# Performance work log

Hardware: AMD Instinct MI355X
Metric: run time of the kernel (lower is better)

## Reference

```python
import jax, jax.numpy as jnp
import numpy as np

B, N, DIM = 16, 1024, 768
H, HD = 12, 64  # num_heads, head_dim


def rotate_half(x):
    x1, x2 = jnp.split(x, 2, axis=-1)
    return jnp.concatenate((-x2, x1), axis=-1)


def setup_inputs() -> dict:
    key = jax.random.key(0)
    k1, k2, k3, k4, k5 = jax.random.split(key, 5)
    x = jax.random.normal(k1, (B, N, DIM), dtype=jnp.float32)
    # precomputed 2D-RoPE angles for the 32x32 patch grid: (N, head_dim)
    sin = jax.random.uniform(k2, (N, HD), dtype=jnp.float32, minval=-1.0, maxval=1.0)
    cos = jax.random.uniform(k3, (N, HD), dtype=jnp.float32, minval=-1.0, maxval=1.0)
    # params: qkv (no bias), proj (with bias)
    W_qkv = jax.random.normal(k4, (DIM, 3 * H * HD), dtype=jnp.float32) / np.sqrt(DIM)
    W_proj = jax.random.normal(k5, (H * HD, DIM), dtype=jnp.float32) / np.sqrt(H * HD)
    b_proj = jnp.zeros((DIM,), dtype=jnp.float32)
    return {"x": x, "sin": sin, "cos": cos, "W_qkv": W_qkv, "W_proj": W_proj, "b_proj": b_proj}


def reference(x, sin, cos, W_qkv, W_proj, b_proj):
    b, n, _ = x.shape
    qkv = (x @ W_qkv).reshape(b, n, 3, H, HD)
    q, k, v = jnp.moveaxis(qkv, 2, 0)          # each (b, n, H, HD)
    q = jnp.swapaxes(q, 1, 2)                  # (b, H, n, HD)
    k = jnp.swapaxes(k, 1, 2)
    v = jnp.swapaxes(v, 1, 2)
    # RoPE (prefix_tokens=0: apply to all tokens); sin/cos broadcast (n,HD)->(1,1,n,HD)
    s = sin[None, None]
    c = cos[None, None]
    q = q * c + rotate_half(q) * s
    k = k * c + rotate_half(k) * s
    # scaled dot-product attention (non-causal, no mask, no dropout)
    scale = 1.0 / jnp.sqrt(jnp.asarray(HD, dtype=q.dtype))
    scores = jnp.einsum('bhqd,bhkd->bhqk', q, k) * scale
    attn = jax.nn.softmax(scores, axis=-1)
    out = jnp.einsum('bhqk,bhkd->bhqd', attn, v)
    out = jnp.swapaxes(out, 1, 2).reshape(b, n, H * HD)
    return out @ W_proj + b_proj
```

## Files before the change

### kernel.cpp

```cpp
#include <hip/hip_runtime.h>


typedef __attribute__((ext_vector_type(8))) _Float16 fp16x8;
typedef __attribute__((ext_vector_type(4))) _Float16 h4;
typedef __attribute__((ext_vector_type(4))) float f32x4;

#define MFMA16(a, b, c) __builtin_amdgcn_mfma_f32_16x16x32_f16(a, b, c, 0, 0, 0)

__device__ __forceinline__ float fexp2(float x) {
    float r;
    asm volatile("v_exp_f32 %0, %1\n\ts_nop 0" : "=v"(r) : "v"(x));
    return r;
}

__device__ __forceinline__ void gload16(const _Float16* g, _Float16* s) {
    __builtin_amdgcn_global_load_lds(
        (const __attribute__((address_space(1))) unsigned int*)g,
        (__attribute__((address_space(3))) unsigned int*)s, 16, 0, 0);
}

__global__ __launch_bounds__(256) void tofp16_kernel(const float* __restrict__ in,
                                                     _Float16* __restrict__ outp, int n4) {
    int i = blockIdx.x * 256 + threadIdx.x;
    if (i >= n4) return;
    float4 v = ((const float4*)in)[i];
    h4 o;
    o[0] = (_Float16)v.x;
    o[1] = (_Float16)v.y;
    o[2] = (_Float16)v.z;
    o[3] = (_Float16)v.w;
    *(h4*)(outp + (size_t)i * 4) = o;
}

__global__ __launch_bounds__(256) void ttrans_kernel(const float* __restrict__ W,
                                                     _Float16* __restrict__ outp,
                                                     int rows, int cols) {
    __shared__ float tile[32][33];
    const int c0 = blockIdx.x * 32, r0 = blockIdx.y * 32;
    const int t = threadIdx.x;
#pragma unroll
    for (int i = 0; i < 4; ++i) {
        int idx = t + i * 256;
        int r = idx >> 5, c = idx & 31;
        tile[r][c] = W[(size_t)(r0 + r) * cols + c0 + c];
    }
    __syncthreads();
#pragma unroll
    for (int i = 0; i < 4; ++i) {
        int idx = t + i * 256;
        int rp = idx >> 5, cp = idx & 31;
        outp[(size_t)(c0 + rp) * rows + r0 + cp] = (_Float16)tile[cp][rp];
    }
}

__global__ __launch_bounds__(256) void ropetab_kernel(const float* __restrict__ sinp,
                                                      const float* __restrict__ cosp,
                                                      float4* __restrict__ tab) {
    int idx = blockIdx.x * 256 + threadIdx.x;
    int n = idx >> 5, d = idx & 31;
    float4 v;
    v.x = cosp[n * 64 + d];
    v.y = sinp[n * 64 + d];
    v.z = cosp[n * 64 + d + 32];
    v.w = sinp[n * 64 + d + 32];
    tab[idx] = v;
}

template <bool SWAP>
__device__ __forceinline__ void gemm_core8(
    const _Float16* __restrict__ Ag, const _Float16* __restrict__ Bg,
    _Float16* lds, int m0, int n0, f32x4 (&acc)[4][4]) {
    constexpr int BUF = 12288;
    constexpr int OB = 8192;
    const int t = threadIdx.x, l = t & 63, w = t >> 6;
    const int wr = w >> 1, wc = w & 1;
    const int hi = l >> 4, qL = l & 15;

    const int scol = ((t & 3) ^ ((t >> 3) & 3)) << 3;
    const int srow = t >> 2;

    int afo[4], bfo[4];
#pragma unroll
    for (int i = 0; i < 4; ++i) {
        int r = wr * 64 + i * 16 + qL;
        afo[i] = r * 32 + ((hi ^ ((r >> 1) & 3)) << 3);
        int c = wc * 64 + i * 16 + qL;
        bfo[i] = OB + c * 32 + ((hi ^ ((c >> 1) & 3)) << 3);
    }

    auto stageA = [&](int kt, int b) {
        _Float16* base = lds + b * BUF;
        const int k0 = kt * 32;
        gload16(Ag + (size_t)(m0 + srow) * 768 + k0 + scol,
                base + (w * 16) * 32);
        gload16(Ag + (size_t)(m0 + 128 + srow) * 768 + k0 + scol,
                base + (128 + w * 16) * 32);
    };
    auto stageB = [&](int kt, int b) {
        _Float16* base = lds + b * BUF;
        const int k0 = kt * 32;
        gload16(Bg + (size_t)(n0 + srow) * 768 + k0 + scol,
                base + OB + (w * 16) * 32);
    };

    stageA(0, 0);
    stageB(0, 0);
    stageA(1, 1);
    stageB(1, 1);
    asm volatile("s_waitcnt vmcnt(3)" ::: "memory");
    __builtin_amdgcn_s_barrier();

    for (int kt = 0; kt < 24; ++kt) {
        const int bn = (kt + 2) % 3;
        _Float16* bb = lds + (kt % 3) * BUF;

        if (kt < 22) stageA(kt + 2, bn);
        fp16x8 af[4], bf[4];
#pragma unroll
        for (int j = 0; j < 4; ++j) bf[j] = *(const fp16x8*)(bb + bfo[j]);
#pragma unroll
        for (int i = 0; i < 2; ++i) af[i] = *(const fp16x8*)(bb + afo[i]);
        __builtin_amdgcn_s_barrier();
        asm volatile("s_waitcnt lgkmcnt(0)" ::: "memory");
        __builtin_amdgcn_s_setprio(1);
#pragma unroll
        for (int i = 0; i < 2; ++i)
#pragma unroll
            for (int j = 0; j < 4; ++j) {
                if constexpr (SWAP)
                    acc[i][j] = MFMA16(bf[j], af[i], acc[i][j]);
                else
                    acc[i][j] = MFMA16(af[i], bf[j], acc[i][j]);
            }
        __builtin_amdgcn_s_setprio(0);
        __builtin_amdgcn_s_barrier();

        if (kt < 22) stageB(kt + 2, bn);
#pragma unroll
        for (int i = 2; i < 4; ++i) af[i] = *(const fp16x8*)(bb + afo[i]);
        __builtin_amdgcn_s_barrier();
        asm volatile("s_waitcnt lgkmcnt(0)" ::: "memory");
        __builtin_amdgcn_s_setprio(1);
#pragma unroll
        for (int i = 2; i < 4; ++i)
#pragma unroll
            for (int j = 0; j < 4; ++j) {
                if constexpr (SWAP)
                    acc[i][j] = MFMA16(bf[j], af[i], acc[i][j]);
                else
                    acc[i][j] = MFMA16(af[i], bf[j], acc[i][j]);
            }
        __builtin_amdgcn_s_setprio(0);

        if (kt < 22)
            asm volatile("s_waitcnt vmcnt(3)" ::: "memory");
        else
            asm volatile("s_waitcnt vmcnt(0)" ::: "memory");
        __builtin_amdgcn_s_barrier();
    }
}

__global__ __launch_bounds__(512, 4) void qkv_qk_gemm(
    const _Float16* __restrict__ Ag, const _Float16* __restrict__ Bg,
    const float4* __restrict__ tab, _Float16* __restrict__ Qf,
    _Float16* __restrict__ Kf) {
    __shared__ _Float16 lds[3 * 12288];
    const int t = threadIdx.x, l = t & 63, w = t >> 6;
    const int wr = w >> 1, wc = w & 1;
    const int hi = l >> 4, qL = l & 15;

    const int bid = blockIdx.x;
    const int xcd = bid & 7, local = bid >> 3;
    const int m0 = (xcd * 8 + (local & 7)) * 256;
    const int n0 = (local >> 3) * 128;

    f32x4 acc[4][4];
#pragma unroll
    for (int i = 0; i < 4; ++i)
#pragma unroll
        for (int j = 0; j < 4; ++j) acc[i][j] = (f32x4){0.f, 0.f, 0.f, 0.f};

    gemm_core8<true>(Ag, Bg, lds, m0, n0, acc);

    const int colbase = n0 + wc * 64;
    const int sector = colbase / 768;
    const int h = (colbase % 768) >> 6;
    _Float16* dst = (sector == 0) ? Qf : Kf;
    const float SC = (sector == 0) ? 0.18033688011f : 1.0f;

#pragma unroll
    for (int ms = 0; ms < 4; ++ms) {
        int m = m0 + wr * 64 + ms * 16 + qL;
        int b = m >> 10, n = m & 1023;
        size_t base = ((size_t)(b * 12 + h) * 1024 + n) * 64;
#pragma unroll
        for (int ns = 0; ns < 2; ++ns) {
            int d0 = ns * 16 + hi * 4;
            h4 lo4, hi4;
#pragma unroll
            for (int reg = 0; reg < 4; ++reg) {
                int d = d0 + reg;
                float4 cs = tab[n * 32 + d];
                float vlo = acc[ms][ns][reg], vhi = acc[ms][ns + 2][reg];
                lo4[reg] = (_Float16)((vlo * cs.x - vhi * cs.y) * SC);
                hi4[reg] = (_Float16)((vhi * cs.z + vlo * cs.w) * SC);
            }
            *(h4*)(dst + base + d0) = lo4;
            *(h4*)(dst + base + d0 + 32) = hi4;
        }
    }
}

__global__ __launch_bounds__(512, 4) void qkv_v_gemm(
    const _Float16* __restrict__ Ag, const _Float16* __restrict__ Bg,
    _Float16* __restrict__ Vt) {
    __shared__ _Float16 lds[3 * 12288];
    const int t = threadIdx.x, l = t & 63, w = t >> 6;
    const int wr = w >> 1, wc = w & 1;
    const int hi = l >> 4, qL = l & 15;

    const int bid = blockIdx.x;
    const int xcd = bid & 7, local = bid >> 3;
    const int m0 = (xcd * 8 + (local & 7)) * 256;
    const int n0 = (12 + (local >> 3)) * 128;

    f32x4 acc[4][4];
#pragma unroll
    for (int i = 0; i < 4; ++i)
#pragma unroll
        for (int j = 0; j < 4; ++j) acc[i][j] = (f32x4){0.f, 0.f, 0.f, 0.f};

    gemm_core8<false>(Ag, Bg, lds, m0, n0, acc);

    const int h = ((n0 + wc * 64) % 768) >> 6;

#pragma unroll
    for (int ms = 0; ms < 4; ++ms) {
        int mbase = m0 + wr * 64 + ms * 16 + hi * 4;
        int b = mbase >> 10, nb = mbase & 1023;
        int bh = b * 12 + h;
#pragma unroll
        for (int ns = 0; ns < 4; ++ns) {
            int d = ns * 16 + qL;
            h4 pk;
#pragma unroll
            for (int reg = 0; reg < 4; ++reg) pk[reg] = (_Float16)acc[ms][ns][reg];
            *(h4*)(Vt + ((size_t)bh * 64 + d) * 1024 + nb) = pk;
        }
    }
}

__global__ __launch_bounds__(512, 4) void proj_gemm(
    const _Float16* __restrict__ Ag, const _Float16* __restrict__ Bg,
    const float* __restrict__ bias, float* __restrict__ out) {
    __shared__ _Float16 lds[3 * 12288];
    const int t = threadIdx.x, l = t & 63, w = t >> 6;
    const int wr = w >> 1, wc = w & 1;
    const int hi = l >> 4, qL = l & 15;

    const int bid = blockIdx.x;
    const int xcd = bid & 7, local = bid >> 3;
    const int m0 = (xcd * 8 + (local & 7)) * 256;
    const int n0 = (local >> 3) * 128;

    f32x4 acc[4][4];
#pragma unroll
    for (int i = 0; i < 4; ++i)
#pragma unroll
        for (int j = 0; j < 4; ++j) acc[i][j] = (f32x4){0.f, 0.f, 0.f, 0.f};

    gemm_core8<true>(Ag, Bg, lds, m0, n0, acc);

#pragma unroll
    for (int ms = 0; ms < 4; ++ms) {
        int m = m0 + wr * 64 + ms * 16 + qL;
#pragma unroll
        for (int ns = 0; ns < 4; ++ns) {
            int c = n0 + wc * 64 + ns * 16 + hi * 4;
            float4 bv = *(const float4*)(bias + c);
            float4 r;
            r.x = acc[ms][ns][0] + bv.x;
            r.y = acc[ms][ns][1] + bv.y;
            r.z = acc[ms][ns][2] + bv.z;
            r.w = acc[ms][ns][3] + bv.w;
            *(float4*)(out + (size_t)m * 768 + c) = r;
        }
    }
}

__global__ __launch_bounds__(256, 3) void attn_kernel(
    const _Float16* __restrict__ Qf, const _Float16* __restrict__ Kfg,
    const _Float16* __restrict__ Vtg, _Float16* __restrict__ aof) {
    __shared__ _Float16 khs[2][64][64];
    __shared__ _Float16 vts[2][64][64];
    __shared__ _Float16 pbuf[4][32][72];

    const int t = threadIdx.x, l = t & 63, w = t >> 6;
    const int flat = blockIdx.x;
    const int xcd = flat & 7, idx = flat >> 3;
    const int bh = xcd * 24 + (idx >> 3);
    const int n0 = (idx & 7) * 128;
    const int bq = bh / 12, hh = bh % 12;
    const size_t base = (size_t)bh << 16;
    const int hi = l >> 4, qL = l & 15;

    fp16x8 qf[2][2];
#pragma unroll
    for (int q2 = 0; q2 < 2; ++q2)
#pragma unroll
        for (int kk = 0; kk < 2; ++kk) {
            size_t off = base + (size_t)(n0 + w * 32 + q2 * 16 + qL) * 64 +
                         kk * 32 + (hi << 3);
            qf[q2][kk] = *(const fp16x8*)(Qf + off);
        }

    const int r0 = w * 16;
    const int srow = l >> 3;
    const int scol = ((l & 7) ^ srow) << 3;
    const _Float16* kf_src = Kfg + base + (size_t)(r0 + srow) * 64 + scol;
    const _Float16* vt_src = Vtg + base + (size_t)(r0 + srow) * 1024 + scol;

    int kfo[4][2];
#pragma unroll
    for (int c = 0; c < 4; ++c)
#pragma unroll
        for (int kk = 0; kk < 2; ++kk) {
            int row = c * 16 + qL;
            int col16 = (kk << 2) | hi;
            kfo[c][kk] = row * 64 + ((col16 ^ (row & 7)) << 3);
        }

    f32x4 ot[4][2];
    float l_part[2] = {0.f, 0.f};
#pragma unroll
    for (int q2 = 0; q2 < 2; ++q2)
#pragma unroll
        for (int dt = 0; dt < 4; ++dt) ot[dt][q2] = (f32x4){0.f, 0.f, 0.f, 0.f};

    auto stage = [&](int kt, int b) {
        const _Float16* ks = kf_src + (size_t)kt * 4096;
        gload16(ks, &khs[b][r0][0]);
        gload16(ks + 512, &khs[b][r0 + 8][0]);
        const _Float16* vs = vt_src + kt * 64;
        gload16(vs, &vts[b][r0][0]);
        gload16(vs + 8 * 1024, &vts[b][r0 + 8][0]);
    };

    stage(0, 0);
    __syncthreads();

    for (int kt = 0; kt < 16; ++kt) {
        const int cur = kt & 1;
        if (kt < 15) stage(kt + 1, cur ^ 1);

        const _Float16* kb = &khs[cur][0][0];
        const _Float16* vb = &vts[cur][0][0];

        f32x4 s[4][2];
#pragma unroll
        for (int c = 0; c < 4; ++c) {
            fp16x8 kf0 = *(const fp16x8*)(kb + kfo[c][0]);
            fp16x8 kf1 = *(const fp16x8*)(kb + kfo[c][1]);
#pragma unroll
            for (int q2 = 0; q2 < 2; ++q2) {
                f32x4 a = (f32x4){0.f, 0.f, 0.f, 0.f};
                a = MFMA16(kf0, qf[q2][0], a);
                a = MFMA16(kf1, qf[q2][1], a);
                s[c][q2] = a;
            }
        }

#pragma unroll
        for (int q2 = 0; q2 < 2; ++q2) {
            const int prow = q2 * 16 + qL;
            float lsum = 0.f;
#pragma unroll
            for (int c = 0; c < 4; ++c) {
                float p0 = fexp2(s[c][q2][0] - 4.0f);
                float p1 = fexp2(s[c][q2][1] - 4.0f);
                float p2 = fexp2(s[c][q2][2] - 4.0f);
                float p3 = fexp2(s[c][q2][3] - 4.0f);
                lsum += (p0 + p1) + (p2 + p3);
                h4 pk;
                pk[0] = (_Float16)p0;
                pk[1] = (_Float16)p1;
                pk[2] = (_Float16)p2;
                pk[3] = (_Float16)p3;
                *(h4*)&pbuf[w][prow][c * 16 + (hi << 2)] = pk;
            }
            l_part[q2] += lsum;
        }

        fp16x8 pf[2][2];
#pragma unroll
        for (int q2 = 0; q2 < 2; ++q2)
#pragma unroll
            for (int ss = 0; ss < 2; ++ss)
                pf[q2][ss] = *(const fp16x8*)&pbuf[w][q2 * 16 + qL][ss * 32 + (hi << 3)];

#pragma unroll
        for (int dt = 0; dt < 4; ++dt) {
            fp16x8 v0 = *(const fp16x8*)(vb + kfo[dt][0]);
            fp16x8 v1 = *(const fp16x8*)(vb + kfo[dt][1]);
#pragma unroll
            for (int q2 = 0; q2 < 2; ++q2) {
                ot[dt][q2] = MFMA16(v0, pf[q2][0], ot[dt][q2]);
                ot[dt][q2] = MFMA16(v1, pf[q2][1], ot[dt][q2]);
            }
        }

        __syncthreads();
    }

#pragma unroll
    for (int q2 = 0; q2 < 2; ++q2) {
        float ls = l_part[q2];
        ls += __shfl_xor(ls, 16);
        ls += __shfl_xor(ls, 32);
        float inv = 1.0f / ls;
        int n = n0 + w * 32 + q2 * 16 + qL;
        size_t rowoff = ((size_t)(bq * 1024 + n)) * 768 + hh * 64 + (hi << 2);
#pragma unroll
        for (int dt = 0; dt < 4; ++dt) {
            h4 r;
#pragma unroll
            for (int reg = 0; reg < 4; ++reg) r[reg] = (_Float16)(ot[dt][q2][reg] * inv);
            *(h4*)(aof + rowoff + dt * 16) = r;
        }
    }
}

extern "C" void kernel_launch(void* const* d_in, const int* in_sizes, int n_in,
                              void* d_out, int out_size, void* d_ws, size_t ws_size,
                              hipStream_t stream) {
    const float* x = (const float*)d_in[0];
    const float* sinp = (const float*)d_in[1];
    const float* cosp = (const float*)d_in[2];
    const float* Wqkv = (const float*)d_in[3];
    const float* Wproj = (const float*)d_in[4];
    const float* bproj = (const float*)d_in[5];
    float* out = (float*)d_out;

    char* ws = (char*)d_ws;
    _Float16* xf  = (_Float16*)(ws);
    _Float16* wqt = (_Float16*)(ws + 25165824);
    _Float16* wpt = (_Float16*)(ws + 28704768);
    _Float16* Qf  = (_Float16*)(ws + 29884416);
    _Float16* Kf  = (_Float16*)(ws + 55050240);
    _Float16* Vt  = (_Float16*)(ws + 80216064);
    float4*   tab = (float4*)(ws + 105381888);
    _Float16* aof = xf;

    tofp16_kernel<<<12288, 256, 0, stream>>>(x, xf, 3145728);
    ttrans_kernel<<<dim3(72, 24), 256, 0, stream>>>(Wqkv, wqt, 768, 2304);
    ttrans_kernel<<<dim3(24, 24), 256, 0, stream>>>(Wproj, wpt, 768, 768);
    ropetab_kernel<<<128, 256, 0, stream>>>(sinp, cosp, tab);
    qkv_qk_gemm<<<768, 512, 0, stream>>>(xf, wqt, tab, Qf, Kf);
    qkv_v_gemm<<<384, 512, 0, stream>>>(xf, wqt, Vt);
    attn_kernel<<<1536, 256, 0, stream>>>(Qf, Kf, Vt, aof);
    proj_gemm<<<384, 512, 0, stream>>>(aof, wpt, bproj, out);
}
```

Baseline: 217.3 us.

## Merge Q/K and V projection GEMMs into one launch, add MFMA priority hints

Result: faster. 203.7 us (-6.2%).

```diff
diff --git a/kernel.cpp b/kernel.cpp
--- a/kernel.cpp
+++ b/kernel.cpp
@@ -160,10 +160,10 @@
     }
 }
 
-__global__ __launch_bounds__(512, 4) void qkv_qk_gemm(
+__global__ __launch_bounds__(512, 4) void qkv_gemm(
     const _Float16* __restrict__ Ag, const _Float16* __restrict__ Bg,
     const float4* __restrict__ tab, _Float16* __restrict__ Qf,
-    _Float16* __restrict__ Kf) {
+    _Float16* __restrict__ Kf, _Float16* __restrict__ Vt) {
     __shared__ _Float16 lds[3 * 12288];
     const int t = threadIdx.x, l = t & 63, w = t >> 6;
     const int wr = w >> 1, wc = w & 1;
@@ -180,72 +180,63 @@
 #pragma unroll
         for (int j = 0; j < 4; ++j) acc[i][j] = (f32x4){0.f, 0.f, 0.f, 0.f};
 
-    gemm_core8<true>(Ag, Bg, lds, m0, n0, acc);
+    gemm_core8<false>(Ag, Bg, lds, m0, n0, acc);
 
     const int colbase = n0 + wc * 64;
     const int sector = colbase / 768;
     const int h = (colbase % 768) >> 6;
-    _Float16* dst = (sector == 0) ? Qf : Kf;
-    const float SC = (sector == 0) ? 0.18033688011f : 1.0f;
-
-#pragma unroll
-    for (int ms = 0; ms < 4; ++ms) {
-        int m = m0 + wr * 64 + ms * 16 + qL;
-        int b = m >> 10, n = m & 1023;
-        size_t base = ((size_t)(b * 12 + h) * 1024 + n) * 64;
-#pragma unroll
-        for (int ns = 0; ns < 2; ++ns) {
-            int d0 = ns * 16 + hi * 4;
-            h4 lo4, hi4;
+    const float SC = 0.18033688011f;
+
+    if (sector == 2) {
+#pragma unroll
+        for (int ms = 0; ms < 4; ++ms) {
+            int mbase = m0 + wr * 64 + ms * 16 + hi * 4;
+            int b = mbase >> 10, nb = mbase & 1023;
+            int bh = b * 12 + h;
+#pragma unroll
+            for (int ns = 0; ns < 4; ++ns) {
+                int d = ns * 16 + qL;
+                h4 pk;
+#pragma unroll
+                for (int reg = 0; reg < 4; ++reg) pk[reg] = (_Float16)acc[ms][ns][reg];
+                *(h4*)(Vt + ((size_t)bh * 64 + d) * 1024 + nb) = pk;
+            }
+        }
+    } else if (sector == 0) {
+#pragma unroll
+        for (int ms = 0; ms < 4; ++ms) {
 #pragma unroll
             for (int reg = 0; reg < 4; ++reg) {
-                int d = d0 + reg;
-                float4 cs = tab[n * 32 + d];
-                float vlo = acc[ms][ns][reg], vhi = acc[ms][ns + 2][reg];
-                lo4[reg] = (_Float16)((vlo * cs.x - vhi * cs.y) * SC);
-                hi4[reg] = (_Float16)((vhi * cs.z + vlo * cs.w) * SC);
-            }
-            *(h4*)(dst + base + d0) = lo4;
-            *(h4*)(dst + base + d0 + 32) = hi4;
-        }
-    }
-}
-
-__global__ __launch_bounds__(512, 4) void qkv_v_gemm(
-    const _Float16* __restrict__ Ag, const _Float16* __restrict__ Bg,
-    _Float16* __restrict__ Vt) {
-    __shared__ _Float16 lds[3 * 12288];
-    const int t = threadIdx.x, l = t & 63, w = t >> 6;
-    const int wr = w >> 1, wc = w & 1;
-    const int hi = l >> 4, qL = l & 15;
-
-    const int bid = blockIdx.x;
-    const int xcd = bid & 7, local = bid >> 3;
-    const int m0 = (xcd * 8 + (local & 7)) * 256;
-    const int n0 = (12 + (local >> 3)) * 128;
-
-    f32x4 acc[4][4];
-#pragma unroll
-    for (int i = 0; i < 4; ++i)
-#pragma unroll
-        for (int j = 0; j < 4; ++j) acc[i][j] = (f32x4){0.f, 0.f, 0.f, 0.f};
-
-    gemm_core8<false>(Ag, Bg, lds, m0, n0, acc);
-
-    const int h = ((n0 + wc * 64) % 768) >> 6;
-
-#pragma unroll
-    for (int ms = 0; ms < 4; ++ms) {
-        int mbase = m0 + wr * 64 + ms * 16 + hi * 4;
-        int b = mbase >> 10, nb = mbase & 1023;
-        int bh = b * 12 + h;
-#pragma unroll
-        for (int ns = 0; ns < 4; ++ns) {
-            int d = ns * 16 + qL;
-            h4 pk;
-#pragma unroll
-            for (int reg = 0; reg < 4; ++reg) pk[reg] = (_Float16)acc[ms][ns][reg];
-            *(h4*)(Vt + ((size_t)bh * 64 + d) * 1024 + nb) = pk;
+                int m = m0 + wr * 64 + ms * 16 + hi * 4 + reg;
+                int b = m >> 10, n = m & 1023;
+                size_t base = ((size_t)(b * 12 + h) * 1024 + n) * 64;
+#pragma unroll
+                for (int p = 0; p < 2; ++p) {
+                    int d = p * 16 + qL;
+                    float4 cs = tab[n * 32 + d];
+                    float vlo = acc[ms][p][reg], vhi = acc[ms][p + 2][reg];
+                    Qf[base + d] = (_Float16)((vlo * cs.x - vhi * cs.y) * SC);
+                    Qf[base + d + 32] = (_Float16)((vhi * cs.z + vlo * cs.w) * SC);
+                }
+            }
+        }
+    } else {
+#pragma unroll
+        for (int ms = 0; ms < 4; ++ms) {
+#pragma unroll
+            for (int reg = 0; reg < 4; ++reg) {
+                int m = m0 + wr * 64 + ms * 16 + hi * 4 + reg;
+                int b = m >> 10, n = m & 1023;
+                size_t base = ((size_t)(b * 12 + h) * 1024 + n) * 64;
+#pragma unroll
+                for (int p = 0; p < 2; ++p) {
+                    int d = p * 16 + qL;
+                    float4 cs = tab[n * 32 + d];
+                    float vlo = acc[ms][p][reg], vhi = acc[ms][p + 2][reg];
+                    Kf[base + d] = (_Float16)(vlo * cs.x - vhi * cs.y);
+                    Kf[base + d + 32] = (_Float16)(vhi * cs.z + vlo * cs.w);
+                }
+            }
         }
     }
 }
@@ -357,6 +348,7 @@
         const _Float16* vb = &vts[cur][0][0];
 
         f32x4 s[4][2];
+        __builtin_amdgcn_s_setprio(1);
 #pragma unroll
         for (int c = 0; c < 4; ++c) {
             fp16x8 kf0 = *(const fp16x8*)(kb + kfo[c][0]);
@@ -369,6 +361,7 @@
                 s[c][q2] = a;
             }
         }
+        __builtin_amdgcn_s_setprio(0);
 
 #pragma unroll
         for (int q2 = 0; q2 < 2; ++q2) {
@@ -398,6 +391,7 @@
             for (int ss = 0; ss < 2; ++ss)
                 pf[q2][ss] = *(const fp16x8*)&pbuf[w][q2 * 16 + qL][ss * 32 + (hi << 3)];
 
+        __builtin_amdgcn_s_setprio(1);
 #pragma unroll
         for (int dt = 0; dt < 4; ++dt) {
             fp16x8 v0 = *(const fp16x8*)(vb + kfo[dt][0]);
@@ -408,6 +402,7 @@
                 ot[dt][q2] = MFMA16(v1, pf[q2][1], ot[dt][q2]);
             }
         }
+        __builtin_amdgcn_s_setprio(0);
 
         __syncthreads();
     }
@@ -455,8 +450,7 @@
     ttrans_kernel<<<dim3(72, 24), 256, 0, stream>>>(Wqkv, wqt, 768, 2304);
     ttrans_kernel<<<dim3(24, 24), 256, 0, stream>>>(Wproj, wpt, 768, 768);
     ropetab_kernel<<<128, 256, 0, stream>>>(sinp, cosp, tab);
-    qkv_qk_gemm<<<768, 512, 0, stream>>>(xf, wqt, tab, Qf, Kf);
-    qkv_v_gemm<<<384, 512, 0, stream>>>(xf, wqt, Vt);
+    qkv_gemm<<<1152, 512, 0, stream>>>(xf, wqt, tab, Qf, Kf, Vt);
     attn_kernel<<<1536, 256, 0, stream>>>(Qf, Kf, Vt, aof);
     proj_gemm<<<384, 512, 0, stream>>>(aof, wpt, bproj, out);
 }
```
